# Performance work log

Measured on AMD Instinct MI355X. Metric: run time of the kernel, lower is better.

## Reference

```python
import jax, jax.numpy as jnp
import numpy as np

B, N, E = 2, 20000, 200000
IN_F, OUT_F, HEADS = 256, 32, 4
NEG_SLOPE = 0.2


def setup_inputs() -> dict:
    key = jax.random.key(0)
    k1, k2, k3, k4 = jax.random.split(key, 4)
    x = jax.random.normal(k1, (B, N, IN_F), dtype=jnp.float32)
    edge_indices = jax.random.randint(k2, (2, E), 0, N, dtype=jnp.int64)
    # xavier-uniform-like scales
    W = jax.random.normal(k3, (OUT_F * HEADS, IN_F), dtype=jnp.float32) * np.float32(1.0 / np.sqrt(IN_F))
    a = jax.random.normal(k4, (2 * OUT_F, 1), dtype=jnp.float32) * np.float32(0.1)
    return {"x": x, "edge_indices": edge_indices, "W": W, "a": a}


def reference(x, edge_indices, W, a):
    Bq, Nq, _ = x.shape
    Hh, Ff = HEADS, OUT_F
    # h: [B, N, H, F]
    h = (x @ W.T).reshape(Bq, Nq, Hh, Ff)
    src, dst = edge_indices[0], edge_indices[1]
    Eq = src.shape[0]
    h_src = h[:, src]  # [B, E, H, F]
    h_dst = h[:, dst]  # [B, E, H, F]
    # scores = leaky_relu(concat(h_src, h_dst) @ a)  without materializing concat
    a_src, a_dst = a[:Ff, 0], a[Ff:, 0]
    scores = (jnp.einsum('behf,f->beh', h_src, a_src)
              + jnp.einsum('behf,f->beh', h_dst, a_dst))
    scores = jnp.where(scores > 0, scores, NEG_SLOPE * scores)  # LeakyReLU(0.2)
    # Original applies softmax over dim=0 (the BATCH dim) per edge
    sm = jax.nn.softmax(scores, axis=0)  # [B, E, H]
    # Original loop overwrites attention_weights[:, src] per edge, so only the
    # LAST edge with a given src survives.
    edge_ids = jnp.arange(Eq, dtype=jnp.int32)
    last_edge = jax.ops.segment_max(edge_ids, src, num_segments=Nq)
    has_edge = jax.ops.segment_sum(jnp.ones((Eq,), jnp.int32), src, num_segments=Nq) > 0
    last_edge = jnp.clip(last_edge, 0, Eq - 1)
    aw = jnp.where(has_edge[None, :, None], sm[:, last_edge], 0.0)  # [B, N, H]
    # aggregated[:, s] = aw[:, s] * sum_{edges i: src[i]==s} h_dst[:, i]
    seg = jax.ops.segment_sum(jnp.transpose(h_dst, (1, 0, 2, 3)), src, num_segments=Nq)  # [N,B,H,F]
    seg = jnp.transpose(seg, (1, 0, 2, 3))  # [B, N, H, F]
    aggregated = aw[..., None] * seg
    # mean over heads; dropout is identity in eval mode
    return aggregated.mean(axis=2)  # [B, N, F]
```

## Files before the change

### kernel.cpp

```cpp
#include <hip/hip_runtime.h>
#include <hip/hip_bf16.h>

#define BB 2
#define NN 20000
#define EE 200000
#define INF 256
#define OUTF 32
#define NH 4
#define HF 128
#define NEG_SLOPE 0.2f
#define GEMM_BLOCKS 1250
#define EDGE_BLOCKS 98
#define CAP 96
#define OVF_CAP 8192

using bf16 = __hip_bfloat16;
typedef __attribute__((ext_vector_type(8))) short bf16x8;
typedef __attribute__((ext_vector_type(4))) float f32x4;

__device__ __forceinline__ float bf2f(unsigned short s){ return __uint_as_float((unsigned)s << 16); }
__device__ __forceinline__ ushort f2bf_bits(float f){
    __hip_bfloat16 b = __float2bfloat16(f);
    return *(ushort*)&b;
}

__device__ __forceinline__ int get_src(const int* ei, int e, int f64){
    return f64 ? ei[2 * e] : ei[e];
}
__device__ __forceinline__ int get_dst(const int* ei, int e, int f64){
    return f64 ? ei[2 * EE + 2 * e] : ei[EE + e];
}

__global__ void k_init(const ushort* __restrict__ xr, const int* __restrict__ er,
                       const void* __restrict__ Wv,
                       int* __restrict__ flags, ushort* __restrict__ wbf,
                       int* __restrict__ cnt, int* __restrict__ last_e,
                       int* __restrict__ ovf_cnt){
    int i = blockIdx.x * blockDim.x + threadIdx.x;
    if (i < NN){ cnt[i] = 0; last_e[i] = -1; }
    if (i == 0) *ovf_cnt = 0;
    if (blockIdx.x == 0){
        __shared__ int cnt_big, cnt_nz;
        if (threadIdx.x == 0){ cnt_big = 0; cnt_nz = 0; }
        __syncthreads();
        int big = 0;
        for (int k = threadIdx.x; k < 8192; k += blockDim.x){
            unsigned e = ((unsigned)xr[2 * k] >> 7) & 0xff;
            if (e >= 0xC0) big++;
        }
        int nz = 0;
        for (int k = threadIdx.x; k < 4096; k += blockDim.x){
            if (er[2 * k + 1] != 0) nz++;
        }
        atomicAdd(&cnt_big, big);
        atomicAdd(&cnt_nz, nz);
        __syncthreads();
        if (threadIdx.x == 0){
            flags[0] = (cnt_big >= 16) ? 1 : 0;
            flags[1] = (cnt_nz == 0) ? 1 : 0;
        }
        const bool f32w = (cnt_big >= 16);
        for (int fr = threadIdx.x; fr < 4096; fr += blockDim.x){
            int lane = fr & 63;
            int t    = (fr >> 6) & 3;
            int kc   = (fr >> 8) & 7;
            int ch   = fr >> 11;
            int col  = ch * 64 + t * 16 + (lane & 15);
            int kb   = kc * 32 + (lane >> 4) * 8;
            bf16x8 v;
            if (f32w){
                const float* wg = (const float*)Wv + (size_t)col * INF + kb;
                #pragma unroll
                for (int j = 0; j < 8; ++j) v[j] = (short)f2bf_bits(wg[j]);
            } else {
                const ushort* wg = (const ushort*)Wv + (size_t)col * INF + kb;
                #pragma unroll
                for (int j = 0; j < 8; ++j) v[j] = (short)wg[j];
            }
            *(bf16x8*)(wbf + (size_t)fr * 8) = v;
        }
    }
}

__global__ __launch_bounds__(256, 4)
void k_gemm(const void* __restrict__ xv_, const ushort* __restrict__ wbf,
            const void* __restrict__ av, const int* __restrict__ ei,
            const int* __restrict__ flags, ushort* __restrict__ h,
            float* __restrict__ alpha_s, float* __restrict__ alpha_d,
            int* __restrict__ last_e, int* __restrict__ cnt,
            ushort* __restrict__ slots, int* __restrict__ ovf_cnt,
            int* __restrict__ ovf_list){
    if (blockIdx.x >= GEMM_BLOCKS){
        int f64 = flags[1];
        int t = (blockIdx.x - GEMM_BLOCKS) * 256 + threadIdx.x;
        for (int e = t; e < EE; e += EDGE_BLOCKS * 256){
            int s = get_src(ei, e, f64);
            int d = get_dst(ei, e, f64);
            atomicMax(&last_e[s], e);
            int idx = atomicAdd(&cnt[s], 1);
            if (idx < CAP) slots[(size_t)s * CAP + idx] = (ushort)d;
            else { int o = atomicAdd(ovf_cnt, 1); if (o < OVF_CAP) ovf_list[o] = e; }
        }
        return;
    }

    const int tid  = threadIdx.x;
    const int lane = tid & 63;
    const int w    = tid >> 6;
    const int l15  = lane & 15;
    const int q    = lane >> 4;
    const bool f32 = flags[0] != 0;

    const int row0 = blockIdx.x * 32 + (w >> 1) * 16;
    const int ch   = w & 1;
    const int hd0  = ch * 2;

    f32x4 acc[4];
    #pragma unroll
    for (int t = 0; t < 4; ++t) acc[t] = (f32x4){0.f, 0.f, 0.f, 0.f};

    const ushort* wb = wbf + (size_t)ch * 16384;

    if (f32){
        const float* xp = (const float*)xv_ + (size_t)(row0 + l15) * INF + q * 8;
        float4 raw[8][2];
        #pragma unroll
        for (int kc = 0; kc < 8; ++kc){
            const float4* p = (const float4*)(xp + kc * 32);
            raw[kc][0] = p[0];
            raw[kc][1] = p[1];
        }
        #pragma unroll
        for (int kc = 0; kc < 8; ++kc){
            float4 lo = raw[kc][0], hi = raw[kc][1];
            bf16x8 afrag;
            afrag[0] = (short)f2bf_bits(lo.x); afrag[1] = (short)f2bf_bits(lo.y);
            afrag[2] = (short)f2bf_bits(lo.z); afrag[3] = (short)f2bf_bits(lo.w);
            afrag[4] = (short)f2bf_bits(hi.x); afrag[5] = (short)f2bf_bits(hi.y);
            afrag[6] = (short)f2bf_bits(hi.z); afrag[7] = (short)f2bf_bits(hi.w);
            #pragma unroll
            for (int t = 0; t < 4; ++t){
                bf16x8 bfrag = *(const bf16x8*)(wb + (((size_t)kc * 4 + t) * 64 + lane) * 8);
                acc[t] = __builtin_amdgcn_mfma_f32_16x16x32_bf16(afrag, bfrag, acc[t], 0, 0, 0);
            }
        }
    } else {
        const ushort* xp = (const ushort*)xv_ + (size_t)(row0 + l15) * INF + q * 8;
        #pragma unroll
        for (int kc = 0; kc < 8; ++kc){
            bf16x8 afrag = *(const bf16x8*)(xp + kc * 32);
            #pragma unroll
            for (int t = 0; t < 4; ++t){
                bf16x8 bfrag = *(const bf16x8*)(wb + (((size_t)kc * 4 + t) * 64 + lane) * 8);
                acc[t] = __builtin_amdgcn_mfma_f32_16x16x32_bf16(afrag, bfrag, acc[t], 0, 0, 0);
            }
        }
    }

    #pragma unroll
    for (int r = 0; r < 4; ++r){
        int row = row0 + q * 4 + r;
        #pragma unroll
        for (int t = 0; t < 2; ++t){
            unsigned v = (unsigned)f2bf_bits(acc[t][r])
                       | ((unsigned)f2bf_bits(acc[t + 2][r]) << 16);
            int f = t * 16 + l15;
            *(unsigned*)(h + (size_t)row * HF + f * 4 + hd0) = v;
        }
    }

    float as_lo, as_hi, ad_lo, ad_hi;
    if (f32){
        const float* af = (const float*)av;
        as_lo = af[l15];        as_hi = af[16 + l15];
        ad_lo = af[OUTF + l15]; ad_hi = af[OUTF + 16 + l15];
    } else {
        const ushort* ab = (const ushort*)av;
        as_lo = bf2f(ab[l15]);        as_hi = bf2f(ab[16 + l15]);
        ad_lo = bf2f(ab[OUTF + l15]); ad_hi = bf2f(ab[OUTF + 16 + l15]);
    }
    #pragma unroll
    for (int r = 0; r < 4; ++r){
        int row = row0 + q * 4 + r;
        #pragma unroll
        for (int hp = 0; hp < 2; ++hp){
            int t0 = hp * 2, t1 = hp * 2 + 1;
            float ps = acc[t0][r] * as_lo + acc[t1][r] * as_hi;
            float pd = acc[t0][r] * ad_lo + acc[t1][r] * ad_hi;
            ps += __shfl_down(ps, 8, 16); pd += __shfl_down(pd, 8, 16);
            ps += __shfl_down(ps, 4, 16); pd += __shfl_down(pd, 4, 16);
            ps += __shfl_down(ps, 2, 16); pd += __shfl_down(pd, 2, 16);
            ps += __shfl_down(ps, 1, 16); pd += __shfl_down(pd, 1, 16);
            if (l15 == 0){
                size_t o = (size_t)row * NH + hd0 + hp;
                alpha_s[o] = ps;
                alpha_d[o] = pd;
            }
        }
    }
}

__global__ void k_aw(const int* __restrict__ ei, const int* __restrict__ flags,
                     const int* __restrict__ last_e,
                     const float* __restrict__ alpha_s, const float* __restrict__ alpha_d,
                     float* __restrict__ aw){
    int n = blockIdx.x * blockDim.x + threadIdx.x;
    if (n >= NN) return;
    int le = last_e[n];
    if (le < 0){
        #pragma unroll
        for (int hh = 0; hh < NH; ++hh){
            aw[((size_t)0 * NN + n) * NH + hh] = 0.f;
            aw[((size_t)1 * NN + n) * NH + hh] = 0.f;
        }
        return;
    }
    int d = get_dst(ei, le, flags[1]);
    #pragma unroll
    for (int hh = 0; hh < NH; ++hh){
        float s0 = alpha_s[((size_t)0 * NN + n) * NH + hh] + alpha_d[((size_t)0 * NN + d) * NH + hh];
        float s1 = alpha_s[((size_t)1 * NN + n) * NH + hh] + alpha_d[((size_t)1 * NN + d) * NH + hh];
        s0 = s0 > 0.f ? s0 : NEG_SLOPE * s0;
        s1 = s1 > 0.f ? s1 : NEG_SLOPE * s1;
        float m  = fmaxf(s0, s1);
        float e0 = __expf(s0 - m);
        float e1 = __expf(s1 - m);
        float inv = 1.f / (e0 + e1);
        aw[((size_t)0 * NN + n) * NH + hh] = 0.25f * e0 * inv;
        aw[((size_t)1 * NN + n) * NH + hh] = 0.25f * e1 * inv;
    }
}

__global__ __launch_bounds__(256)
void k_agg(const ushort* __restrict__ slots, const int* __restrict__ cnt,
           const ushort* __restrict__ h, const float* __restrict__ aw,
           float* __restrict__ out_f){
    int lane = threadIdx.x & 63;
    int wid  = (blockIdx.x * blockDim.x + threadIdx.x) >> 6;
    int nw   = (gridDim.x * blockDim.x) >> 6;
    int b = lane >> 5;
    int f = lane & 31;
    for (int n = wid; n < NN; n += nw){
        int m = cnt[n]; if (m > CAP) m = CAP;
        const ushort* sl = slots + (size_t)n * CAP;
        const ushort* hb = h + (size_t)b * NN * HF + f * 4;
        float ax = 0.f, ay = 0.f, az = 0.f, aww = 0.f;
        int i = 0;
        for (; i + 4 <= m; i += 4){
            ushort4 dd = *(const ushort4*)(sl + i);
            ushort4 u0 = *(const ushort4*)(hb + (size_t)dd.x * HF);
            ushort4 u1 = *(const ushort4*)(hb + (size_t)dd.y * HF);
            ushort4 u2 = *(const ushort4*)(hb + (size_t)dd.z * HF);
            ushort4 u3 = *(const ushort4*)(hb + (size_t)dd.w * HF);
            ax += bf2f(u0.x) + bf2f(u1.x) + bf2f(u2.x) + bf2f(u3.x);
            ay += bf2f(u0.y) + bf2f(u1.y) + bf2f(u2.y) + bf2f(u3.y);
            az += bf2f(u0.z) + bf2f(u1.z) + bf2f(u2.z) + bf2f(u3.z);
            aww += bf2f(u0.w) + bf2f(u1.w) + bf2f(u2.w) + bf2f(u3.w);
        }
        for (; i < m; ++i){
            ushort4 u = *(const ushort4*)(hb + (size_t)sl[i] * HF);
            ax += bf2f(u.x); ay += bf2f(u.y); az += bf2f(u.z); aww += bf2f(u.w);
        }
        float4 awv = *(const float4*)(aw + ((size_t)b * NN + n) * NH);
        out_f[((size_t)b * NN + n) * OUTF + f] =
            awv.x * ax + awv.y * ay + awv.z * az + awv.w * aww;
    }
}

__global__ void k_fix(const int* __restrict__ ei, const int* __restrict__ flags,
                      const int* __restrict__ ovf_cnt, const int* __restrict__ ovf_list,
                      const ushort* __restrict__ h, const float* __restrict__ aw,
                      float* __restrict__ out_f){
    int lane = threadIdx.x & 63;
    int wid  = (blockIdx.x * blockDim.x + threadIdx.x) >> 6;
    int nw   = (gridDim.x * blockDim.x) >> 6;
    int b = lane >> 5;
    int f = lane & 31;
    int M = *ovf_cnt; if (M > OVF_CAP) M = OVF_CAP;
    int f64 = flags[1];
    for (int i = wid; i < M; i += nw){
        int e = ovf_list[i];
        int s = get_src(ei, e, f64);
        int d = get_dst(ei, e, f64);
        float4 awv = *(const float4*)(aw + ((size_t)b * NN + s) * NH);
        ushort4 u = *(const ushort4*)(h + ((size_t)b * NN + d) * HF + f * 4);
        float acc = awv.x * bf2f(u.x) + awv.y * bf2f(u.y)
                  + awv.z * bf2f(u.z) + awv.w * bf2f(u.w);
        atomicAdd(&out_f[((size_t)b * NN + s) * OUTF + f], acc);
    }
}

extern "C" void kernel_launch(void* const* d_in, const int* in_sizes, int n_in,
                              void* d_out, int out_size, void* d_ws, size_t ws_size,
                              hipStream_t stream){
    const void* x = d_in[0]; const void* eiv = d_in[1];
    const void* W = d_in[2]; const void* a  = d_in[3];
    for (int i = 0; i < n_in; ++i){
        if      (in_sizes[i] == BB * NN * INF) x   = d_in[i];
        else if (in_sizes[i] == 2 * EE)        eiv = d_in[i];
        else if (in_sizes[i] == HF * INF)      W   = d_in[i];
        else if (in_sizes[i] == 2 * OUTF)      a   = d_in[i];
    }
    const int* ei = (const int*)eiv;
    float* out = (float*)d_out;

    const size_t HN = (size_t)BB * NN * HF;
    char* p = (char*)d_ws;
    int*    flags    = (int*)p;                       p += 64;
    ushort* wbf      = (ushort*)p;                    p += 32768 * 2;
    ushort* h        = (ushort*)p;                    p += HN * 2;
    float*  alpha_s  = (float*)p;                     p += (size_t)BB * NN * NH * 4;
    float*  alpha_d  = (float*)p;                     p += (size_t)BB * NN * NH * 4;
    float*  aw       = (float*)p;                     p += (size_t)BB * NN * NH * 4;
    int*    last_e   = (int*)p;                       p += (size_t)NN * 4;
    int*    cnt      = (int*)p;                       p += (size_t)NN * 4;
    int*    ovf_cnt  = (int*)p;                       p += 64;
    int*    ovf_list = (int*)p;                       p += (size_t)OVF_CAP * 4;
    ushort* slots    = (ushort*)p;

    k_init <<<(NN + 255) / 256, 256, 0, stream>>>((const ushort*)x, ei, W, flags, wbf,
                                                  cnt, last_e, ovf_cnt);
    k_gemm <<<GEMM_BLOCKS + EDGE_BLOCKS, 256, 0, stream>>>(x, wbf, a, ei, flags, h,
                                                           alpha_s, alpha_d, last_e,
                                                           cnt, slots, ovf_cnt, ovf_list);
    k_aw   <<<(NN + 255) / 256, 256, 0, stream>>>(ei, flags, last_e, alpha_s, alpha_d, aw);
    k_agg  <<<2048, 256, 0, stream>>>(slots, cnt, h, aw, out);
    k_fix  <<<32, 256, 0, stream>>>(ei, flags, ovf_cnt, ovf_list, h, aw, out);
}
```

Measured before the change: 153.5 us.

## Fuse attention-weight kernel into aggregation, widen GEMM tiles, parallelize edge and weight prep

The separate k_aw kernel is removed, and each aggregation wave now computes the per-node batch softmax weights itself, sharing them across lanes with shuffles. It still writes aw for the overflow fix-up kernel. In the GEMM, each wave now computes all four heads for 16 rows, reusing the A fragment across both weight halves and storing h with 8-byte writes. Edge binning now uses one thread per edge and runs first in the grid, and weight repacking is spread over 16 blocks. The aim is to cut one launch and intermediate traffic, and to overlap edge binning better. The cost is more accumulator registers per wave and redundant flag-sampling work in each of the 16 init blocks.

```diff
diff --git a/kernel.cpp b/kernel.cpp
--- a/kernel.cpp
+++ b/kernel.cpp
@@ -9,8 +9,8 @@
 #define NH 4
 #define HF 128
 #define NEG_SLOPE 0.2f
-#define GEMM_BLOCKS 1250
-#define EDGE_BLOCKS 98
+#define GEMM_BLOCKS 625
+#define EDGE_BLOCKS 782
 #define CAP 96
 #define OVF_CAP 8192
 
@@ -39,7 +39,7 @@
     int i = blockIdx.x * blockDim.x + threadIdx.x;
     if (i < NN){ cnt[i] = 0; last_e[i] = -1; }
     if (i == 0) *ovf_cnt = 0;
-    if (blockIdx.x == 0){
+    if (blockIdx.x < 16){
         __shared__ int cnt_big, cnt_nz;
         if (threadIdx.x == 0){ cnt_big = 0; cnt_nz = 0; }
         __syncthreads();
@@ -55,12 +55,13 @@
         atomicAdd(&cnt_big, big);
         atomicAdd(&cnt_nz, nz);
         __syncthreads();
-        if (threadIdx.x == 0){
+        if (blockIdx.x == 0 && threadIdx.x == 0){
             flags[0] = (cnt_big >= 16) ? 1 : 0;
             flags[1] = (cnt_nz == 0) ? 1 : 0;
         }
         const bool f32w = (cnt_big >= 16);
-        for (int fr = threadIdx.x; fr < 4096; fr += blockDim.x){
+        int fr = blockIdx.x * 256 + threadIdx.x;
+        {
             int lane = fr & 63;
             int t    = (fr >> 6) & 3;
             int kc   = (fr >> 8) & 7;
@@ -90,10 +91,10 @@
             int* __restrict__ last_e, int* __restrict__ cnt,
             ushort* __restrict__ slots, int* __restrict__ ovf_cnt,
             int* __restrict__ ovf_list){
-    if (blockIdx.x >= GEMM_BLOCKS){
+    if (blockIdx.x < EDGE_BLOCKS){
         int f64 = flags[1];
-        int t = (blockIdx.x - GEMM_BLOCKS) * 256 + threadIdx.x;
-        for (int e = t; e < EE; e += EDGE_BLOCKS * 256){
+        int e = blockIdx.x * 256 + threadIdx.x;
+        if (e < EE){
             int s = get_src(ei, e, f64);
             int d = get_dst(ei, e, f64);
             atomicMax(&last_e[s], e);
@@ -104,6 +105,7 @@
         return;
     }
 
+    const int bid  = blockIdx.x - EDGE_BLOCKS;
     const int tid  = threadIdx.x;
     const int lane = tid & 63;
     const int w    = tid >> 6;
@@ -111,15 +113,13 @@
     const int q    = lane >> 4;
     const bool f32 = flags[0] != 0;
 
-    const int row0 = blockIdx.x * 32 + (w >> 1) * 16;
-    const int ch   = w & 1;
-    const int hd0  = ch * 2;
-
-    f32x4 acc[4];
+    const int row0 = bid * 64 + w * 16;
+
+    f32x4 acc[2][4];
     #pragma unroll
-    for (int t = 0; t < 4; ++t) acc[t] = (f32x4){0.f, 0.f, 0.f, 0.f};
-
-    const ushort* wb = wbf + (size_t)ch * 16384;
+    for (int c = 0; c < 2; ++c)
+        #pragma unroll
+        for (int t = 0; t < 4; ++t) acc[c][t] = (f32x4){0.f, 0.f, 0.f, 0.f};
 
     if (f32){
         const float* xp = (const float*)xv_ + (size_t)(row0 + l15) * INF + q * 8;
@@ -139,9 +139,13 @@
             afrag[4] = (short)f2bf_bits(hi.x); afrag[5] = (short)f2bf_bits(hi.y);
             afrag[6] = (short)f2bf_bits(hi.z); afrag[7] = (short)f2bf_bits(hi.w);
             #pragma unroll
-            for (int t = 0; t < 4; ++t){
-                bf16x8 bfrag = *(const bf16x8*)(wb + (((size_t)kc * 4 + t) * 64 + lane) * 8);
-                acc[t] = __builtin_amdgcn_mfma_f32_16x16x32_bf16(afrag, bfrag, acc[t], 0, 0, 0);
+            for (int c = 0; c < 2; ++c){
+                const ushort* wb = wbf + (size_t)c * 16384;
+                #pragma unroll
+                for (int t = 0; t < 4; ++t){
+                    bf16x8 bfrag = *(const bf16x8*)(wb + (((size_t)kc * 4 + t) * 64 + lane) * 8);
+                    acc[c][t] = __builtin_amdgcn_mfma_f32_16x16x32_bf16(afrag, bfrag, acc[c][t], 0, 0, 0);
+                }
             }
         }
     } else {
@@ -150,9 +154,13 @@
         for (int kc = 0; kc < 8; ++kc){
             bf16x8 afrag = *(const bf16x8*)(xp + kc * 32);
             #pragma unroll
-            for (int t = 0; t < 4; ++t){
-                bf16x8 bfrag = *(const bf16x8*)(wb + (((size_t)kc * 4 + t) * 64 + lane) * 8);
-                acc[t] = __builtin_amdgcn_mfma_f32_16x16x32_bf16(afrag, bfrag, acc[t], 0, 0, 0);
+            for (int c = 0; c < 2; ++c){
+                const ushort* wb = wbf + (size_t)c * 16384;
+                #pragma unroll
+                for (int t = 0; t < 4; ++t){
+                    bf16x8 bfrag = *(const bf16x8*)(wb + (((size_t)kc * 4 + t) * 64 + lane) * 8);
+                    acc[c][t] = __builtin_amdgcn_mfma_f32_16x16x32_bf16(afrag, bfrag, acc[c][t], 0, 0, 0);
+                }
             }
         }
     }
@@ -162,10 +170,13 @@
         int row = row0 + q * 4 + r;
         #pragma unroll
         for (int t = 0; t < 2; ++t){
-            unsigned v = (unsigned)f2bf_bits(acc[t][r])
-                       | ((unsigned)f2bf_bits(acc[t + 2][r]) << 16);
+            unsigned v0 = (unsigned)f2bf_bits(acc[0][t][r])
+                        | ((unsigned)f2bf_bits(acc[0][t + 2][r]) << 16);
+            unsigned v1 = (unsigned)f2bf_bits(acc[1][t][r])
+                        | ((unsigned)f2bf_bits(acc[1][t + 2][r]) << 16);
             int f = t * 16 + l15;
-            *(unsigned*)(h + (size_t)row * HF + f * 4 + hd0) = v;
+            uint2 vv; vv.x = v0; vv.y = v1;
+            *(uint2*)(h + (size_t)row * HF + f * 4) = vv;
         }
     }
 
@@ -183,65 +194,67 @@
     for (int r = 0; r < 4; ++r){
         int row = row0 + q * 4 + r;
         #pragma unroll
-        for (int hp = 0; hp < 2; ++hp){
-            int t0 = hp * 2, t1 = hp * 2 + 1;
-            float ps = acc[t0][r] * as_lo + acc[t1][r] * as_hi;
-            float pd = acc[t0][r] * ad_lo + acc[t1][r] * ad_hi;
-            ps += __shfl_down(ps, 8, 16); pd += __shfl_down(pd, 8, 16);
-            ps += __shfl_down(ps, 4, 16); pd += __shfl_down(pd, 4, 16);
-            ps += __shfl_down(ps, 2, 16); pd += __shfl_down(pd, 2, 16);
-            ps += __shfl_down(ps, 1, 16); pd += __shfl_down(pd, 1, 16);
-            if (l15 == 0){
-                size_t o = (size_t)row * NH + hd0 + hp;
-                alpha_s[o] = ps;
-                alpha_d[o] = pd;
+        for (int c = 0; c < 2; ++c){
+            #pragma unroll
+            for (int hp = 0; hp < 2; ++hp){
+                int t0 = hp * 2, t1 = hp * 2 + 1;
+                float ps = acc[c][t0][r] * as_lo + acc[c][t1][r] * as_hi;
+                float pd = acc[c][t0][r] * ad_lo + acc[c][t1][r] * ad_hi;
+                ps += __shfl_down(ps, 8, 16); pd += __shfl_down(pd, 8, 16);
+                ps += __shfl_down(ps, 4, 16); pd += __shfl_down(pd, 4, 16);
+                ps += __shfl_down(ps, 2, 16); pd += __shfl_down(pd, 2, 16);
+                ps += __shfl_down(ps, 1, 16); pd += __shfl_down(pd, 1, 16);
+                if (l15 == 0){
+                    size_t o = (size_t)row * NH + c * 2 + hp;
+                    alpha_s[o] = ps;
+                    alpha_d[o] = pd;
+                }
             }
         }
-    }
-}
-
-__global__ void k_aw(const int* __restrict__ ei, const int* __restrict__ flags,
-                     const int* __restrict__ last_e,
-                     const float* __restrict__ alpha_s, const float* __restrict__ alpha_d,
-                     float* __restrict__ aw){
-    int n = blockIdx.x * blockDim.x + threadIdx.x;
-    if (n >= NN) return;
-    int le = last_e[n];
-    if (le < 0){
-        #pragma unroll
-        for (int hh = 0; hh < NH; ++hh){
-            aw[((size_t)0 * NN + n) * NH + hh] = 0.f;
-            aw[((size_t)1 * NN + n) * NH + hh] = 0.f;
-        }
-        return;
-    }
-    int d = get_dst(ei, le, flags[1]);
-    #pragma unroll
-    for (int hh = 0; hh < NH; ++hh){
-        float s0 = alpha_s[((size_t)0 * NN + n) * NH + hh] + alpha_d[((size_t)0 * NN + d) * NH + hh];
-        float s1 = alpha_s[((size_t)1 * NN + n) * NH + hh] + alpha_d[((size_t)1 * NN + d) * NH + hh];
-        s0 = s0 > 0.f ? s0 : NEG_SLOPE * s0;
-        s1 = s1 > 0.f ? s1 : NEG_SLOPE * s1;
-        float m  = fmaxf(s0, s1);
-        float e0 = __expf(s0 - m);
-        float e1 = __expf(s1 - m);
-        float inv = 1.f / (e0 + e1);
-        aw[((size_t)0 * NN + n) * NH + hh] = 0.25f * e0 * inv;
-        aw[((size_t)1 * NN + n) * NH + hh] = 0.25f * e1 * inv;
     }
 }
 
 __global__ __launch_bounds__(256)
 void k_agg(const ushort* __restrict__ slots, const int* __restrict__ cnt,
-           const ushort* __restrict__ h, const float* __restrict__ aw,
+           const int* __restrict__ last_e, const int* __restrict__ ei,
+           const int* __restrict__ flags,
+           const float* __restrict__ alpha_s, const float* __restrict__ alpha_d,
+           const ushort* __restrict__ h, float* __restrict__ aw,
            float* __restrict__ out_f){
     int lane = threadIdx.x & 63;
     int wid  = (blockIdx.x * blockDim.x + threadIdx.x) >> 6;
     int nw   = (gridDim.x * blockDim.x) >> 6;
     int b = lane >> 5;
     int f = lane & 31;
+    int c  = lane & 7;
+    int bb = c >> 2;
+    int hh = c & 3;
+    int f64 = flags[1];
     for (int n = wid; n < NN; n += nw){
-        int m = cnt[n]; if (m > CAP) m = CAP;
+        int m  = cnt[n]; if (m > CAP) m = CAP;
+        int le = last_e[n];
+
+        float my_aw = 0.f;
+        if (le >= 0){
+            int d = get_dst(ei, le, f64);
+            float ss = alpha_s[((size_t)bb * NN + n) * NH + hh]
+                     + alpha_d[((size_t)bb * NN + d) * NH + hh];
+            float so = alpha_s[((size_t)(1 - bb) * NN + n) * NH + hh]
+                     + alpha_d[((size_t)(1 - bb) * NN + d) * NH + hh];
+            ss = ss > 0.f ? ss : NEG_SLOPE * ss;
+            so = so > 0.f ? so : NEG_SLOPE * so;
+            float mx = fmaxf(ss, so);
+            float e0 = __expf(ss - mx);
+            float e1 = __expf(so - mx);
+            my_aw = 0.25f * e0 / (e0 + e1);
+        }
+        if (lane < 8) aw[((size_t)bb * NN + n) * NH + hh] = my_aw;
+
+        float aw0 = __shfl(my_aw, (b << 2) + 0, 8);
+        float aw1 = __shfl(my_aw, (b << 2) + 1, 8);
+        float aw2 = __shfl(my_aw, (b << 2) + 2, 8);
+        float aw3 = __shfl(my_aw, (b << 2) + 3, 8);
+
         const ushort* sl = slots + (size_t)n * CAP;
         const ushort* hb = h + (size_t)b * NN * HF + f * 4;
         float ax = 0.f, ay = 0.f, az = 0.f, aww = 0.f;
@@ -261,9 +274,8 @@
             ushort4 u = *(const ushort4*)(hb + (size_t)sl[i] * HF);
             ax += bf2f(u.x); ay += bf2f(u.y); az += bf2f(u.z); aww += bf2f(u.w);
         }
-        float4 awv = *(const float4*)(aw + ((size_t)b * NN + n) * NH);
         out_f[((size_t)b * NN + n) * OUTF + f] =
-            awv.x * ax + awv.y * ay + awv.z * az + awv.w * aww;
+            aw0 * ax + aw1 * ay + aw2 * az + aw3 * aww;
     }
 }
 
@@ -320,10 +332,10 @@
 
     k_init <<<(NN + 255) / 256, 256, 0, stream>>>((const ushort*)x, ei, W, flags, wbf,
                                                   cnt, last_e, ovf_cnt);
-    k_gemm <<<GEMM_BLOCKS + EDGE_BLOCKS, 256, 0, stream>>>(x, wbf, a, ei, flags, h,
+    k_gemm <<<EDGE_BLOCKS + GEMM_BLOCKS, 256, 0, stream>>>(x, wbf, a, ei, flags, h,
                                                            alpha_s, alpha_d, last_e,
                                                            cnt, slots, ovf_cnt, ovf_list);
-    k_aw   <<<(NN + 255) / 256, 256, 0, stream>>>(ei, flags, last_e, alpha_s, alpha_d, aw);
-    k_agg  <<<2048, 256, 0, stream>>>(slots, cnt, h, aw, out);
+    k_agg  <<<2048, 256, 0, stream>>>(slots, cnt, last_e, ei, flags,
+                                      alpha_s, alpha_d, h, aw, out);
     k_fix  <<<32, 256, 0, stream>>>(ei, flags, ovf_cnt, ovf_list, h, aw, out);
 }
```

Measured after the change: 154.2 us. About the same (+0.4%).
